# Optimization experiments

Measured on AMD Instinct MI355X. Metric: run time of the kernel, lower is better.

Reference implementation:

```python
import jax, jax.numpy as jnp
import numpy as np

EMBED = 1024
HEADS = 16
HEAD_DIM = EMBED // HEADS


def setup_inputs() -> dict:
    key = jax.random.key(0)
    ks = jax.random.split(key, 9)
    B, S = 2, 2048
    values = jax.random.normal(ks[0], (B, S, EMBED), dtype=jnp.float32)
    keys_in = jax.random.normal(ks[1], (B, S, EMBED), dtype=jnp.float32)
    query = jax.random.normal(ks[2], (B, S, EMBED), dtype=jnp.float32)
    mask = jax.random.randint(ks[3], (B, 1, 1, S), 0, 2, dtype=jnp.int32)
    # torch Linear weights: [out_features, in_features], y = x @ W.T
    sc = 1.0 / np.sqrt(HEAD_DIM)
    Wv = jax.random.uniform(ks[4], (HEAD_DIM, HEAD_DIM), jnp.float32, -sc, sc)
    Wk = jax.random.uniform(ks[5], (HEAD_DIM, HEAD_DIM), jnp.float32, -sc, sc)
    Wq = jax.random.uniform(ks[6], (HEAD_DIM, HEAD_DIM), jnp.float32, -sc, sc)
    so = 1.0 / np.sqrt(EMBED)
    Wo = jax.random.uniform(ks[7], (EMBED, EMBED), jnp.float32, -so, so)
    bo = jax.random.uniform(ks[8], (EMBED,), jnp.float32, -so, so)
    return {"values": values, "keys": keys_in, "query": query, "mask": mask,
            "Wv": Wv, "Wk": Wk, "Wq": Wq, "Wo": Wo, "bo": bo}


def reference(values, keys, query, mask, Wv, Wk, Wq, Wo, bo):
    B = query.shape[0]
    # split heads: [B, S, H, D]
    v = values.reshape(B, -1, HEADS, HEAD_DIM)
    k = keys.reshape(B, -1, HEADS, HEAD_DIM)
    q = query.reshape(B, -1, HEADS, HEAD_DIM)
    # per-head shared linear projections (nn.Linear on last dim, no bias)
    v = jnp.einsum('bshd,ed->bshe', v, Wv)
    k = jnp.einsum('bshd,ed->bshe', k, Wk)
    q = jnp.einsum('bshd,ed->bshe', q, Wq)
    # energy: [B, H, Q, K]
    energy = jnp.einsum('bqhd,bkhd->bhqk', q, k)
    energy = jnp.where(mask == 0, jnp.float32(-1e20), energy)
    attn = jax.nn.softmax(energy / jnp.sqrt(jnp.float32(EMBED)), axis=3)
    out = jnp.einsum('bhqk,bkhd->bqhd', attn, v).reshape(B, -1, EMBED)
    return out @ Wo.T + bo
```

## Files before the change

### kernel.cpp

```cpp
#include <hip/hip_runtime.h>
#include <hip/hip_bf16.h>


typedef __attribute__((ext_vector_type(8))) short bf16x8;
typedef __attribute__((ext_vector_type(4))) float f32x4;
typedef __attribute__((ext_vector_type(16))) float f32x16;
typedef __attribute__((ext_vector_type(2))) int i32x2;

__device__ int g_srcidx[2 * 2048];
__device__ int g_NK[2];

__device__ __forceinline__ short f2bf(float x) {
  union { float f; unsigned u; } v; v.f = x;
  unsigned r = v.u + 0x7FFFu + ((v.u >> 16) & 1u);
  return (short)(r >> 16);
}

__device__ __forceinline__ int pack2(float lo, float hi) {
  __hip_bfloat162 h = __float22bfloat162_rn(make_float2(lo, hi));
  int r; __builtin_memcpy(&r, &h, 4); return r;
}

__device__ __forceinline__ bf16x8 cvt8(float4 a, float4 b) {
  union { int i[4]; bf16x8 h; } u;
  u.i[0] = pack2(a.x, a.y);
  u.i[1] = pack2(a.z, a.w);
  u.i[2] = pack2(b.x, b.y);
  u.i[3] = pack2(b.z, b.w);
  return u.h;
}

__device__ __forceinline__ void plsw(int& a, int& b) {
  i32x2 r = __builtin_amdgcn_permlane32_swap(a, b, false, false);
  a = r[0]; b = r[1];
}
__device__ __forceinline__ float pl_comb_add(float v) {
  int a = __float_as_int(v), b = a;
  i32x2 r = __builtin_amdgcn_permlane32_swap(a, b, false, false);
  return __int_as_float(r[0]) + __int_as_float(r[1]);
}

__device__ __forceinline__ void gll16(const short* g, short* l) {
  __builtin_amdgcn_global_load_lds(
      (const __attribute__((address_space(1))) void*)g,
      (__attribute__((address_space(3))) void*)l, 16, 0, 0);
}

__global__ __launch_bounds__(256) void prep_kernel(
    const int* __restrict__ mask, const float* __restrict__ Wo,
    short* __restrict__ WoB) {
  __shared__ int cnt[256];
  const int t = threadIdx.x;
  if (blockIdx.x < 2) {
    const int b = blockIdx.x;
    const int* m = mask + b * 2048;
    int* sidx = g_srcidx + b * 2048;
    const int base = t * 8;
    int vals[8], lc = 0;
#pragma unroll
    for (int i = 0; i < 8; i++) { vals[i] = (m[base + i] != 0); lc += vals[i]; }
    cnt[t] = lc;
    __syncthreads();
    for (int off = 1; off < 256; off <<= 1) {
      int v = (t >= off) ? cnt[t - off] : 0;
      __syncthreads();
      cnt[t] += v;
      __syncthreads();
    }
    int pos = cnt[t] - lc;
    const int total = cnt[255];
#pragma unroll
    for (int i = 0; i < 8; i++)
      if (vals[i]) sidx[pos++] = base + i;
    for (int j = total + t; j < 2048; j += 256) sidx[j] = 0;
    if (t == 0) g_NK[b] = total;
  } else {
    int i = ((blockIdx.x - 2) * 256 + t) * 8;
    float4 a = *(const float4*)(Wo + i), b2 = *(const float4*)(Wo + i + 4);
    *(bf16x8*)(WoB + i) = cvt8(a, b2);
  }
}

__global__ __launch_bounds__(256) void proj_kernel(
    const float* __restrict__ keys, const float* __restrict__ query,
    const float* __restrict__ values,
    const float* __restrict__ Wk, const float* __restrict__ Wq,
    const float* __restrict__ Wv,
    short* __restrict__ Kp, short* __restrict__ Qp, short* __restrict__ Vt) {
  const int bid0 = blockIdx.x;
  const int t = threadIdx.x;
  const int w = t >> 6, l = t & 63, l15 = l & 15, l4 = l >> 4;
  __shared__ short Al[64 * 64];
  __shared__ short Bl[64 * 64];
  __shared__ short Tl[64 * 66];

  if (bid0 < 2048) {
    int bid = bid0;
    const float* X = keys; const float* W = Wk; short* O = Kp;
    bool isq = false;
    if (bid >= 1024) { X = query; W = Wq; O = Qp; bid -= 1024; isq = true; }
    const int r0 = bid << 6;
    const int bb = r0 >> 15;
    if (!isq) {
      const int j0 = (r0 >> 4) & 2047;
      const int jlim = (g_NK[bb] + 63) & ~63;
      if (j0 >= jlim) return;
    }
#pragma unroll
    for (int i = 0; i < 2; i++) {
      int c = t + (i << 8);
      int row = c >> 3, col8 = c & 7;
      int pc = col8 ^ (row & 7);
      int ri = r0 + row;
      int j = (ri >> 4) & 2047, hh = ri & 15;
      int s = isq ? j : g_srcidx[(bb << 11) + j];
      const float* xs = X + ((size_t)((bb * 2048 + s) * 16 + hh)) * 64 + col8 * 8;
      float4 a0 = *(const float4*)xs, a1 = *(const float4*)(xs + 4);
      *(bf16x8*)&Al[row * 64 + pc * 8] = cvt8(a0, a1);
      const float* wsrc = W + row * 64 + col8 * 8;
      float4 b0 = *(const float4*)wsrc, b1 = *(const float4*)(wsrc + 4);
      *(bf16x8*)&Bl[row * 64 + pc * 8] = cvt8(b0, b1);
    }
    __syncthreads();
    f32x4 acc[4];
#pragma unroll
    for (int i = 0; i < 4; i++) acc[i] = (f32x4){0.f, 0.f, 0.f, 0.f};
#pragma unroll
    for (int kc = 0; kc < 2; kc++) {
      int ar = w * 16 + l15;
      bf16x8 af = *(const bf16x8*)((const char*)Al +
          ((ar * 128 + kc * 64 + l4 * 16) ^ ((ar & 7) << 4)));
#pragma unroll
      for (int ng = 0; ng < 4; ng++) {
        int br = ng * 16 + l15;
        bf16x8 bfr = *(const bf16x8*)((const char*)Bl +
            ((br * 128 + kc * 64 + l4 * 16) ^ ((br & 7) << 4)));
        acc[ng] = __builtin_amdgcn_mfma_f32_16x16x32_bf16(af, bfr, acc[ng], 0, 0, 0);
      }
    }
    const float osc = isq ? (1.4426950408889634f / 32.0f) : 1.0f;
#pragma unroll
    for (int ng = 0; ng < 4; ng++) {
#pragma unroll
      for (int j = 0; j < 4; j++) {
        int ri = r0 + w * 16 + l4 * 4 + j;
        int e = ng * 16 + l15;
        int b2 = ri >> 15, jj = (ri >> 4) & 2047, hh = ri & 15;
        O[(((size_t)(b2 * 16 + hh)) * 2048 + jj) * 64 + e] = f2bf(acc[ng][j] * osc);
      }
    }
  } else {
    const int bid = bid0 - 2048;
    const int st = bid & 31, bh = bid >> 5;
    const int b = bh >> 4, h = bh & 15;
    const int s0 = st << 6;
    const int jlim = (g_NK[b] + 63) & ~63;
    if (s0 >= jlim) return;
#pragma unroll
    for (int i = 0; i < 2; i++) {
      int c = t + (i << 8);
      int row = c >> 3, col8 = c & 7;
      int pc = col8 ^ (row & 7);
      int s = g_srcidx[(b << 11) + s0 + row];
      const float* xs = values + ((size_t)(b * 2048 + s)) * 1024 + h * 64 + col8 * 8;
      float4 a0 = *(const float4*)xs, a1 = *(const float4*)(xs + 4);
      *(bf16x8*)&Al[row * 64 + pc * 8] = cvt8(a0, a1);
      const float* wsrc = Wv + row * 64 + col8 * 8;
      float4 b0 = *(const float4*)wsrc, b1 = *(const float4*)(wsrc + 4);
      *(bf16x8*)&Bl[row * 64 + pc * 8] = cvt8(b0, b1);
    }
    __syncthreads();
    f32x4 acc[4];
#pragma unroll
    for (int i = 0; i < 4; i++) acc[i] = (f32x4){0.f, 0.f, 0.f, 0.f};
#pragma unroll
    for (int kc = 0; kc < 2; kc++) {
      int ar = w * 16 + l15;
      bf16x8 af = *(const bf16x8*)((const char*)Al +
          ((ar * 128 + kc * 64 + l4 * 16) ^ ((ar & 7) << 4)));
#pragma unroll
      for (int ng = 0; ng < 4; ng++) {
        int br = ng * 16 + l15;
        bf16x8 bfr = *(const bf16x8*)((const char*)Bl +
            ((br * 128 + kc * 64 + l4 * 16) ^ ((br & 7) << 4)));
        acc[ng] = __builtin_amdgcn_mfma_f32_16x16x32_bf16(af, bfr, acc[ng], 0, 0, 0);
      }
    }
#pragma unroll
    for (int ng = 0; ng < 4; ng++) {
#pragma unroll
      for (int j = 0; j < 4; j++) {
        Tl[(w * 16 + l4 * 4 + j) * 66 + ng * 16 + l15] = f2bf(acc[ng][j]);
      }
    }
    __syncthreads();
    int e = t >> 2, sc = (t & 3) << 4;
    bf16x8 o0, o1;
#pragma unroll
    for (int i = 0; i < 8; i++) {
      o0[i] = Tl[(sc + i) * 66 + e];
      o1[i] = Tl[(sc + 8 + i) * 66 + e];
    }
    short* dst = Vt + ((size_t)bh * 64 + e) * 2048 + s0 + sc;
    *(bf16x8*)dst = o0;
    *(bf16x8*)(dst + 8) = o1;
  }
}

__global__ __launch_bounds__(256, 2) void attn_kernel(
    const short* __restrict__ Qp, const short* __restrict__ Kp,
    const short* __restrict__ Vt, short* __restrict__ AO) {
  const int bid = blockIdx.x;
  const int qb = bid & 15, bh = bid >> 4;
  const int b = bh >> 4, h = bh & 15;
  const int t = threadIdx.x;
  const int w = t >> 6, l = t & 63, l31 = l & 31, hi = l >> 5;
  const int q0w = qb * 128 + w * 32;

  __shared__ short Kl[4][64 * 64];
  __shared__ short Vl[4][64 * 64];
  __shared__ float Cl[4 * 32];

  const short* Kbase = Kp + (size_t)bh * 2048 * 64;
  const short* Vbase = Vt + (size_t)bh * 64 * 2048;

  const int nk = g_NK[b];
  const int ntiles = (nk + 63) >> 6;

  const short* qptr = Qp + ((size_t)bh * 2048 + q0w + l31) * 64 + hi * 8;
  bf16x8 qf[4];
#pragma unroll
  for (int dc = 0; dc < 4; dc++) qf[dc] = *(const bf16x8*)(qptr + dc * 16);

  int laddr[2][4];
#pragma unroll
  for (int x = 0; x < 2; x++) {
    int rr = x * 32 + l31;
#pragma unroll
    for (int c2 = 0; c2 < 4; c2++)
      laddr[x][c2] = rr * 128 + (((c2 * 32) + hi * 16) ^ ((rr & 7) << 4));
  }

  const int srow = t >> 3, scol = t & 7;
  const int sc0 = (scol ^ (srow & 7)) * 8;
  const short* ksrc0 = Kbase + srow * 64 + sc0;
  const short* ksrc1 = Kbase + (srow + 32) * 64 + sc0;
  const short* vsrc0 = Vbase + (size_t)srow * 2048 + sc0;
  const short* vsrc1 = Vbase + (size_t)(srow + 32) * 2048 + sc0;
  short* klds = &Kl[0][0];
  short* vlds = &Vl[0][0];
  const int d0 = t * 8, d1 = t * 8 + 2048;

  float l_run = 0.f;
  f32x16 o0, o1;
#pragma unroll
  for (int r = 0; r < 16; r++) { o0[r] = 0.f; o1[r] = 0.f; }

  auto stage = [&](int kt, int bufi) {
    const int off = bufi << 12;
    gll16(ksrc0 + kt * 4096, klds + off + d0);
    gll16(ksrc1 + kt * 4096, klds + off + d1);
    gll16(vsrc0 + kt * 64, vlds + off + d0);
    gll16(vsrc1 + kt * 64, vlds + off + d1);
  };

  auto compute = [&](int kt, int bufi) {
    const int bsb = bufi << 13;
    f32x16 st0, st1;
#pragma unroll
    for (int r = 0; r < 16; r++) { st0[r] = 0.f; st1[r] = 0.f; }
    __builtin_amdgcn_s_setprio(1);
#pragma unroll
    for (int dc = 0; dc < 4; dc++) {
      bf16x8 ka = *(const bf16x8*)((const char*)Kl + bsb + laddr[0][dc]);
      st0 = __builtin_amdgcn_mfma_f32_32x32x16_bf16(ka, qf[dc], st0, 0, 0, 0);
    }
#pragma unroll
    for (int dc = 0; dc < 4; dc++) {
      bf16x8 kb = *(const bf16x8*)((const char*)Kl + bsb + laddr[1][dc]);
      st1 = __builtin_amdgcn_mfma_f32_32x32x16_bf16(kb, qf[dc], st1, 0, 0, 0);
    }
    __builtin_amdgcn_s_setprio(0);

    if (((kt << 6) + 64) <= nk) {
#pragma unroll
      for (int r = 0; r < 16; r++) {
        st0[r] = __builtin_amdgcn_exp2f(st0[r]);
        st1[r] = __builtin_amdgcn_exp2f(st1[r]);
      }
    } else {
      const int kb2 = kt << 6;
#pragma unroll
      for (int r = 0; r < 16; r++) {
        int cr = (r & 3) + 8 * (r >> 2) + 4 * hi;
        float e0 = __builtin_amdgcn_exp2f(st0[r]);
        float e1 = __builtin_amdgcn_exp2f(st1[r]);
        st0[r] = (kb2 + cr < nk) ? e0 : 0.f;
        st1[r] = (kb2 + 32 + cr < nk) ? e1 : 0.f;
      }
    }

    float sx[8];
#pragma unroll
    for (int i = 0; i < 8; i++)
      sx[i] = (st0[2 * i] + st0[2 * i + 1]) + (st1[2 * i] + st1[2 * i + 1]);
#pragma unroll
    for (int s2 = 4; s2 > 0; s2 >>= 1)
#pragma unroll
      for (int i = 0; i < 4; i++)
        if (i < s2) sx[i] += sx[i + s2];
    l_run += pl_comb_add(sx[0]);

    bf16x8 pa[4];
#pragma unroll
    for (int kc = 0; kc < 4; kc++) {
      int bse = (kc & 1) * 8;
      float p0, p1, p2, p3, p4, p5, p6, p7;
      if (kc < 2) {
        p0 = st0[bse + 0]; p1 = st0[bse + 1]; p2 = st0[bse + 2]; p3 = st0[bse + 3];
        p4 = st0[bse + 4]; p5 = st0[bse + 5]; p6 = st0[bse + 6]; p7 = st0[bse + 7];
      } else {
        p0 = st1[bse + 0]; p1 = st1[bse + 1]; p2 = st1[bse + 2]; p3 = st1[bse + 3];
        p4 = st1[bse + 4]; p5 = st1[bse + 5]; p6 = st1[bse + 6]; p7 = st1[bse + 7];
      }
      int A0 = pack2(p0, p1), A1 = pack2(p2, p3);
      int B0 = pack2(p4, p5), B1 = pack2(p6, p7);
      plsw(A0, B0);
      plsw(A1, B1);
      union { int4 i; bf16x8 h; } u;
      u.i = make_int4(A0, A1, B0, B1);
      pa[kc] = u.h;
    }

    __builtin_amdgcn_s_setprio(1);
#pragma unroll
    for (int kc = 0; kc < 4; kc++) {
      bf16x8 vf = *(const bf16x8*)((const char*)Vl + bsb + laddr[0][kc]);
      o0 = __builtin_amdgcn_mfma_f32_32x32x16_bf16(pa[kc], vf, o0, 0, 0, 0);
    }
#pragma unroll
    for (int kc = 0; kc < 4; kc++) {
      bf16x8 vf = *(const bf16x8*)((const char*)Vl + bsb + laddr[1][kc]);
      o1 = __builtin_amdgcn_mfma_f32_32x32x16_bf16(pa[kc], vf, o1, 0, 0, 0);
    }
    __builtin_amdgcn_s_setprio(0);
  };

  stage(0, 0);
  if (ntiles > 1) stage(1, 1);
  __syncthreads();

  for (int kt = 0; kt < ntiles; kt += 2) {
    const int p = (kt >> 1) & 1;
    const int cb = p * 2;
    const int nb = (1 - p) * 2;
    if (kt + 2 < ntiles) stage(kt + 2, nb);
    if (kt + 3 < ntiles) stage(kt + 3, nb + 1);
    compute(kt, cb);
    if (kt + 1 < ntiles) compute(kt + 1, cb + 1);
    __syncthreads();
  }

  float invr = 1.0f / l_run;
  Cl[w * 32 + l31] = invr;
  short* aob = AO + ((size_t)(b * 2048 + q0w)) * 1024 + h * 64 + l31;
#pragma unroll
  for (int r = 0; r < 16; r++) {
    int qr = (r & 3) + 8 * (r >> 2) + 4 * hi;
    float ic = Cl[w * 32 + qr];
    aob[(size_t)qr * 1024] = f2bf(o0[r] * ic);
    aob[(size_t)qr * 1024 + 32] = f2bf(o1[r] * ic);
  }
}

__global__ __launch_bounds__(256) void outproj_kernel(
    const short* __restrict__ AO, const short* __restrict__ WoB,
    const float* __restrict__ bo, float* __restrict__ Cout) {
  const int bid = blockIdx.x;
  const int mt = bid >> 4, nt = bid & 15;
  const int m0 = mt << 6, n0 = nt << 6;
  const int t = threadIdx.x;
  const int w = t >> 6, l = t & 63, l15 = l & 15, l4 = l >> 4;
  __shared__ short Al[2][64 * 64];
  __shared__ short Bl[2][64 * 64];

  const int srow = t >> 3, scol = t & 7;
  const int sc0 = (scol ^ (srow & 7)) * 8;
  const short* asrc0 = AO + (size_t)(m0 + srow) * 1024 + sc0;
  const short* asrc1 = AO + (size_t)(m0 + srow + 32) * 1024 + sc0;
  const short* bsrc0 = WoB + (size_t)(n0 + srow) * 1024 + sc0;
  const short* bsrc1 = WoB + (size_t)(n0 + srow + 32) * 1024 + sc0;
  short* al = &Al[0][0];
  short* bl = &Bl[0][0];
  const int d0 = t * 8, d1 = t * 8 + 2048;

  gll16(asrc0, al + d0); gll16(asrc1, al + d1);
  gll16(bsrc0, bl + d0); gll16(bsrc1, bl + d1);
  __syncthreads();

  f32x4 acc[4];
#pragma unroll
  for (int i = 0; i < 4; i++) acc[i] = (f32x4){0.f, 0.f, 0.f, 0.f};

  for (int ks = 0; ks < 16; ks++) {
    const int bs = ks & 1, bsb = bs << 13;
    if (ks < 15) {
      const int nb = (bs ^ 1) << 12;
      const int ko = (ks + 1) * 64;
      gll16(asrc0 + ko, al + nb + d0); gll16(asrc1 + ko, al + nb + d1);
      gll16(bsrc0 + ko, bl + nb + d0); gll16(bsrc1 + ko, bl + nb + d1);
    }
#pragma unroll
    for (int kc = 0; kc < 2; kc++) {
      int ar = w * 16 + l15;
      bf16x8 af = *(const bf16x8*)((const char*)Al + bsb +
          ((ar * 128 + kc * 64 + l4 * 16) ^ ((ar & 7) << 4)));
#pragma unroll
      for (int ng = 0; ng < 4; ng++) {
        int br = ng * 16 + l15;
        bf16x8 bfr = *(const bf16x8*)((const char*)Bl + bsb +
            ((br * 128 + kc * 64 + l4 * 16) ^ ((br & 7) << 4)));
        acc[ng] = __builtin_amdgcn_mfma_f32_16x16x32_bf16(af, bfr, acc[ng], 0, 0, 0);
      }
    }
    __syncthreads();
  }
#pragma unroll
  for (int ng = 0; ng < 4; ng++) {
    int n = n0 + ng * 16 + l15;
    float bias = bo[n];
#pragma unroll
    for (int j = 0; j < 4; j++) {
      int m = m0 + w * 16 + l4 * 4 + j;
      Cout[(size_t)m * 1024 + n] = acc[ng][j] + bias;
    }
  }
}

extern "C" void kernel_launch(void* const* d_in, const int* in_sizes, int n_in,
                              void* d_out, int out_size, void* d_ws, size_t ws_size,
                              hipStream_t stream) {
  const float* values = (const float*)d_in[0];
  const float* keys   = (const float*)d_in[1];
  const float* query  = (const float*)d_in[2];
  const int*   mask   = (const int*)d_in[3];
  const float* Wv = (const float*)d_in[4];
  const float* Wk = (const float*)d_in[5];
  const float* Wq = (const float*)d_in[6];
  const float* Wo = (const float*)d_in[7];
  const float* bo = (const float*)d_in[8];
  float* out = (float*)d_out;
  char* ws = (char*)d_ws;
  short* Qp  = (short*)(ws + (size_t)0);
  short* Kp  = (short*)(ws + ((size_t)8 << 20));
  short* Vtp = (short*)(ws + ((size_t)16 << 20));
  short* AO  = (short*)(ws + ((size_t)24 << 20));
  short* WoB = (short*)(ws + ((size_t)32 << 20));

  prep_kernel<<<514, 256, 0, stream>>>(mask, Wo, WoB);
  proj_kernel<<<3072, 256, 0, stream>>>(keys, query, values, Wk, Wq, Wv, Kp, Qp, Vtp);
  attn_kernel<<<512, 256, 0, stream>>>(Qp, Kp, Vtp, AO);
  outproj_kernel<<<1024, 256, 0, stream>>>(AO, WoB, bo, out);
}
```

Before: 70.57 us.

## Split attention key tiles across two warp groups and reduce partials in LDS

Doubles the attention block to 512 threads. Two groups of four waves each process alternating key tiles for the same 128 queries. Each half of the block stages one tile of the double-buffered pair, and at the end the second group's partial O and row sums are added into the first group's through shared memory. The aim is more waves per CU to hide latency and a shorter serial loop over key tiles. The costs are an extra LDS reduction, and possible register pressure or spilling from the tighter launch bound of (512, 4).

```diff
diff --git a/kernel.cpp b/kernel.cpp
--- a/kernel.cpp
+++ b/kernel.cpp
@@ -207,15 +207,16 @@
   }
 }
 
-__global__ __launch_bounds__(256, 2) void attn_kernel(
+__global__ __launch_bounds__(512, 4) void attn_kernel(
     const short* __restrict__ Qp, const short* __restrict__ Kp,
     const short* __restrict__ Vt, short* __restrict__ AO) {
   const int bid = blockIdx.x;
   const int qb = bid & 15, bh = bid >> 4;
   const int b = bh >> 4, h = bh & 15;
   const int t = threadIdx.x;
-  const int w = t >> 6, l = t & 63, l31 = l & 31, hi = l >> 5;
-  const int q0w = qb * 128 + w * 32;
+  const int w = t >> 6, wq = w & 3, wg = w >> 2;
+  const int l = t & 63, l31 = l & 31, hi = l >> 5;
+  const int q0w = qb * 128 + wq * 32;
 
   __shared__ short Kl[4][64 * 64];
   __shared__ short Vl[4][64 * 64];
@@ -241,7 +242,8 @@
       laddr[x][c2] = rr * 128 + (((c2 * 32) + hi * 16) ^ ((rr & 7) << 4));
   }
 
-  const int srow = t >> 3, scol = t & 7;
+  const int sh = t >> 8, tt = t & 255;
+  const int srow = tt >> 3, scol = tt & 7;
   const int sc0 = (scol ^ (srow & 7)) * 8;
   const short* ksrc0 = Kbase + srow * 64 + sc0;
   const short* ksrc1 = Kbase + (srow + 32) * 64 + sc0;
@@ -249,19 +251,22 @@
   const short* vsrc1 = Vbase + (size_t)(srow + 32) * 2048 + sc0;
   short* klds = &Kl[0][0];
   short* vlds = &Vl[0][0];
-  const int d0 = t * 8, d1 = t * 8 + 2048;
+  const int d0 = tt * 8, d1 = tt * 8 + 2048;
 
   float l_run = 0.f;
   f32x16 o0, o1;
 #pragma unroll
   for (int r = 0; r < 16; r++) { o0[r] = 0.f; o1[r] = 0.f; }
 
-  auto stage = [&](int kt, int bufi) {
-    const int off = bufi << 12;
-    gll16(ksrc0 + kt * 4096, klds + off + d0);
-    gll16(ksrc1 + kt * 4096, klds + off + d1);
-    gll16(vsrc0 + kt * 64, vlds + off + d0);
-    gll16(vsrc1 + kt * 64, vlds + off + d1);
+  auto stage2 = [&](int ktbase) {
+    const int kt = ktbase + sh;
+    if (kt < ntiles) {
+      const int off = ((((ktbase >> 1) & 1) << 1) + sh) << 12;
+      gll16(ksrc0 + kt * 4096, klds + off + d0);
+      gll16(ksrc1 + kt * 4096, klds + off + d1);
+      gll16(vsrc0 + kt * 64, vlds + off + d0);
+      gll16(vsrc1 + kt * 64, vlds + off + d1);
+    }
   };
 
   auto compute = [&](int kt, int bufi) {
@@ -346,28 +351,41 @@
     __builtin_amdgcn_s_setprio(0);
   };
 
-  stage(0, 0);
-  if (ntiles > 1) stage(1, 1);
+  stage2(0);
   __syncthreads();
 
   for (int kt = 0; kt < ntiles; kt += 2) {
+    stage2(kt + 2);
     const int p = (kt >> 1) & 1;
-    const int cb = p * 2;
-    const int nb = (1 - p) * 2;
-    if (kt + 2 < ntiles) stage(kt + 2, nb);
-    if (kt + 3 < ntiles) stage(kt + 3, nb + 1);
-    compute(kt, cb);
-    if (kt + 1 < ntiles) compute(kt + 1, cb + 1);
-    __syncthreads();
+    const int myt = kt + wg;
+    if (myt < ntiles) compute(myt, p * 2 + wg);
+    __syncthreads();
+  }
+
+  float* OL = (float*)&Kl[0][0];
+  float* LL = (float*)&Vl[0][0];
+  if (wg == 1) {
+    float* op = OL + wq * 2048 + l * 32;
+#pragma unroll
+    for (int r = 0; r < 16; r++) { op[r] = o0[r]; op[16 + r] = o1[r]; }
+    LL[wq * 64 + l] = l_run;
+  }
+  __syncthreads();
+  if (wg == 1) return;
+  {
+    float* op = OL + wq * 2048 + l * 32;
+#pragma unroll
+    for (int r = 0; r < 16; r++) { o0[r] += op[r]; o1[r] += op[16 + r]; }
+    l_run += LL[wq * 64 + l];
   }
 
   float invr = 1.0f / l_run;
-  Cl[w * 32 + l31] = invr;
+  Cl[wq * 32 + l31] = invr;
   short* aob = AO + ((size_t)(b * 2048 + q0w)) * 1024 + h * 64 + l31;
 #pragma unroll
   for (int r = 0; r < 16; r++) {
     int qr = (r & 3) + 8 * (r >> 2) + 4 * hi;
-    float ic = Cl[w * 32 + qr];
+    float ic = Cl[wq * 32 + qr];
     aob[(size_t)qr * 1024] = f2bf(o0[r] * ic);
     aob[(size_t)qr * 1024 + 32] = f2bf(o1[r] * ic);
   }
@@ -459,6 +477,6 @@
 
   prep_kernel<<<514, 256, 0, stream>>>(mask, Wo, WoB);
   proj_kernel<<<3072, 256, 0, stream>>>(keys, query, values, Wk, Wq, Wv, Kp, Qp, Vtp);
-  attn_kernel<<<512, 256, 0, stream>>>(Qp, Kp, Vtp, AO);
+  attn_kernel<<<512, 512, 0, stream>>>(Qp, Kp, Vtp, AO);
   outproj_kernel<<<1024, 256, 0, stream>>>(AO, WoB, bo, out);
 }
```

Measured after the change: 73.81 us. +4.6%, slower.
